# Kernel tuning notes

Hardware: AMD Instinct MI355X
Metric: run time of the kernel (lower is better)

The kernel has to match this reference:

```python
import jax, jax.numpy as jnp
import numpy as np

B, S, D = 4, 2048, 1024

def setup_inputs() -> dict:
    key = jax.random.key(0)
    ks = jax.random.split(key, 9)
    sc = 1.0 / np.sqrt(D)
    return {
        "x": jax.random.normal(ks[0], (B, S, D), dtype=jnp.float32),
        "Wq": jax.random.normal(ks[1], (D, D), dtype=jnp.float32) * sc,
        "bq": jnp.zeros((D,), dtype=jnp.float32),
        "Wk": jax.random.normal(ks[2], (D, D), dtype=jnp.float32) * sc,
        "bk": jnp.zeros((D,), dtype=jnp.float32),
        "Wv": jax.random.normal(ks[3], (D, D), dtype=jnp.float32) * sc,
        "bv": jnp.zeros((D,), dtype=jnp.float32),
        "Wo": jax.random.normal(ks[4], (D, D), dtype=jnp.float32) * sc,
        "bo": jnp.zeros((D,), dtype=jnp.float32),
    }

def _gaussian_mask(seq_len, dtype):
    # exp(-0.5*((pos - S/2)/(S/4))^2), shape [1,1,S] -> broadcasts over KEY axis
    pos = jnp.arange(seq_len, dtype=dtype)
    center = seq_len / 2
    sigma = seq_len / 4
    m = jnp.exp(-0.5 * ((pos - center) / sigma) ** 2)
    return m[None, None, :]

def reference(x, Wq, bq, Wk, bk, Wv, bv, Wo, bo):
    d = x.shape[-1]
    Q = x @ Wq.T + bq            # [B,S,D]
    K = x @ Wk.T + bk
    V = x @ Wv.T + bv
    scores = jnp.einsum('bqd,bkd->bqk', Q, K) / jnp.sqrt(jnp.asarray(d, x.dtype))
    scores = scores * _gaussian_mask(x.shape[1], x.dtype)
    attn = jax.nn.softmax(scores, axis=-1)
    out = jnp.einsum('bqk,bkd->bqd', attn, V)
    return out @ Wo.T + bo
```

## Files before the change

kernel.cpp:

```cpp
#include <hip/hip_runtime.h>
#include <math.h>

#define SEQ 2048
#define DIM 1024

typedef __attribute__((ext_vector_type(8))) _Float16 half8;
typedef __attribute__((ext_vector_type(4))) float f32x4;

__device__ __forceinline__ unsigned short f2h(float f) {
    union { _Float16 h; unsigned short u; } c; c.h = (_Float16)f;
    return c.u;
}
__device__ __forceinline__ float gmask(int k) {
    float t = ((float)k - 1024.0f) * (1.0f / 512.0f);
    return expf(-0.5f * t * t);
}
__device__ __forceinline__ void glds16(const unsigned short* gp, unsigned short* lp) {
    __builtin_amdgcn_global_load_lds((const __attribute__((address_space(1))) void*)gp,
                                     (__attribute__((address_space(3))) void*)lp, 16, 0, 0);
}

__device__ __forceinline__ void stage64(const unsigned short* __restrict__ g, int ldK,
                                        unsigned short* lds, int wave, int lane) {
    int row = wave * 32 + (lane >> 3);
    int seg = (lane & 7) ^ (lane >> 3);
    const unsigned short* gp = g + (long)row * ldK + seg * 8;
    unsigned short* lp = lds + wave * 2048;
    glds16(gp, lp);
    glds16(gp + 8 * (long)ldK, lp + 512);
    glds16(gp + 16 * (long)ldK, lp + 1024);
    glds16(gp + 24 * (long)ldK, lp + 1536);
}

enum { EPI_QKV = 0, EPI_EXP = 1, EPI_PV = 2, EPI_OUT = 3 };

template <int EPI>
__global__ __launch_bounds__(256, 2) void mfma_gemm(
    const unsigned short* __restrict__ A, const unsigned short* __restrict__ Bm,
    const float* __restrict__ bias, const float* __restrict__ rs,
    float* __restrict__ Cf, unsigned short* __restrict__ Ch,
    int M, int N, int K, float scale, long sA, long sB, long sC)
{
    __shared__ unsigned short As[128 * 64];
    __shared__ unsigned short Bs[128 * 64];

    const int bz = blockIdx.z;
    const int tid = threadIdx.x;
    const int wave = tid >> 6;
    const int lane = tid & 63;
    const int wm = (wave & 1) * 64;
    const int wn = (wave >> 1) * 64;
    const long m0 = (long)blockIdx.y * 128;
    const long n0 = (long)blockIdx.x * 128;
    const int lm = lane & 15;
    const int lk = lane >> 4;

    const unsigned short* pA = A + bz * sA + m0 * K;
    const unsigned short* pB = Bm + bz * sB + n0 * K;

    f32x4 acc[4][4];
#pragma unroll
    for (int i = 0; i < 4; ++i)
#pragma unroll
        for (int j = 0; j < 4; ++j) {
            acc[i][j].x = 0.f; acc[i][j].y = 0.f; acc[i][j].z = 0.f; acc[i][j].w = 0.f;
        }

    int aoff[4][2], boff[4][2];
#pragma unroll
    for (int i = 0; i < 4; ++i)
#pragma unroll
        for (int t = 0; t < 2; ++t) {
            int ar = wm + i * 16 + lm;
            aoff[i][t] = ar * 64 + (((4 * t + lk) ^ (ar & 7)) << 3);
            int br = wn + i * 16 + lm;
            boff[i][t] = br * 64 + (((4 * t + lk) ^ (br & 7)) << 3);
        }

    for (int k0 = 0; k0 < K; k0 += 64) {
        stage64(pA + k0, K, As, wave, lane);
        stage64(pB + k0, K, Bs, wave, lane);
        __syncthreads();
#pragma unroll
        for (int t = 0; t < 2; ++t) {
            half8 a[4], b[4];
#pragma unroll
            for (int i = 0; i < 4; ++i) a[i] = *(const half8*)(As + aoff[i][t]);
#pragma unroll
            for (int j = 0; j < 4; ++j) b[j] = *(const half8*)(Bs + boff[j][t]);
#pragma unroll
            for (int i = 0; i < 4; ++i)
#pragma unroll
                for (int j = 0; j < 4; ++j)
                    acc[i][j] = __builtin_amdgcn_mfma_f32_16x16x32_f16(a[i], b[j], acc[i][j], 0, 0, 0);
        }
        __syncthreads();
    }

    const long MD = 8388608;
    const float* rsb = (EPI == EPI_PV) ? rs + bz * SEQ : (const float*)nullptr;
    float* cF = (EPI == EPI_OUT) ? Cf + bz * sC : (float*)nullptr;
    unsigned short* cH = (EPI != EPI_OUT) ? Ch + bz * sC : (unsigned short*)nullptr;

#pragma unroll
    for (int i = 0; i < 4; ++i) {
        long mrow = m0 + wm + i * 16 + lk * 4;
        float rs4[4];
        if (EPI == EPI_PV) {
#pragma unroll
            for (int r = 0; r < 4; ++r) rs4[r] = rsb[mrow + r];
        }
#pragma unroll
        for (int j = 0; j < 4; ++j) {
            int n = (int)n0 + wn + j * 16 + lm;
            if (EPI == EPI_QKV) {
                int sel = n >> 10;
                int n1 = n & 1023;
                float bs = bias[n];
                if (sel < 2) {
                    unsigned short* dst = cH + (long)sel * MD;
#pragma unroll
                    for (int r = 0; r < 4; ++r)
                        dst[(mrow + r) * (long)DIM + n1] = f2h(acc[i][j][r] + bs);
                } else {
                    long b = mrow >> 11, s = mrow & 2047;
                    long idx = 2 * MD + b * (long)DIM * SEQ + (long)n1 * SEQ + s;
                    unsigned long long pk =
                        (unsigned long long)f2h(acc[i][j].x + bs) |
                        ((unsigned long long)f2h(acc[i][j].y + bs) << 16) |
                        ((unsigned long long)f2h(acc[i][j].z + bs) << 32) |
                        ((unsigned long long)f2h(acc[i][j].w + bs) << 48);
                    *(unsigned long long*)(cH + idx) = pk;
                }
            } else if (EPI == EPI_EXP) {
                float mult = scale * gmask(n);
#pragma unroll
                for (int r = 0; r < 4; ++r)
                    cH[(mrow + r) * (long)N + n] = f2h(expf(acc[i][j][r] * mult));
            } else if (EPI == EPI_PV) {
#pragma unroll
                for (int r = 0; r < 4; ++r)
                    cH[(mrow + r) * (long)N + n] = f2h(acc[i][j][r] * rs4[r]);
            } else {
                float bs = bias[n];
#pragma unroll
                for (int r = 0; r < 4; ++r)
                    cF[(mrow + r) * (long)N + n] = acc[i][j][r] + bs;
            }
        }
    }
}

__global__ __launch_bounds__(256) void rowsum(const unsigned short* __restrict__ E,
                                              float* __restrict__ invrs)
{
    long base = ((long)blockIdx.y * SEQ + blockIdx.x) * SEQ;
    const int tid = threadIdx.x;
    half8 h = ((const half8*)(E + base))[tid];
    float s = 0.f;
#pragma unroll
    for (int i = 0; i < 8; ++i) s += (float)h[i];
#pragma unroll
    for (int off = 32; off > 0; off >>= 1) s += __shfl_down(s, off);
    __shared__ float red[4];
    if ((tid & 63) == 0) red[tid >> 6] = s;
    __syncthreads();
    if (tid == 0)
        invrs[(long)blockIdx.y * SEQ + blockIdx.x] = 1.0f / (red[0] + red[1] + red[2] + red[3]);
}

__global__ __launch_bounds__(256) void cvt_f16(const float* __restrict__ src,
    unsigned short* __restrict__ dst, long n)
{
    long i = ((long)blockIdx.x * 256 + threadIdx.x) * 4;
    long stride = (long)gridDim.x * 1024;
    for (; i < n; i += stride) {
        float4 v = *(const float4*)(src + i);
        unsigned long long p = (unsigned long long)f2h(v.x) | ((unsigned long long)f2h(v.y) << 16) |
                               ((unsigned long long)f2h(v.z) << 32) | ((unsigned long long)f2h(v.w) << 48);
        *(unsigned long long*)(dst + i) = p;
    }
}

__global__ __launch_bounds__(256) void pack_w4(const float* __restrict__ W0,
    const float* __restrict__ W1, const float* __restrict__ W2, const float* __restrict__ W3,
    unsigned short* __restrict__ dst)
{
    const long WW = 1048576;
    long i = ((long)blockIdx.x * 256 + threadIdx.x) * 4;
    int sel = (int)(i >> 20);
    const float* src = (sel == 0) ? W0 : (sel == 1) ? W1 : (sel == 2) ? W2 : W3;
    float4 v = *(const float4*)(src + (i & (WW - 1)));
    unsigned long long p = (unsigned long long)f2h(v.x) | ((unsigned long long)f2h(v.y) << 16) |
                           ((unsigned long long)f2h(v.z) << 32) | ((unsigned long long)f2h(v.w) << 48);
    *(unsigned long long*)(dst + i) = p;
}

__global__ __launch_bounds__(256) void pack_bias(const float* __restrict__ b0,
    const float* __restrict__ b1, const float* __restrict__ b2, float* __restrict__ dst)
{
    int i = blockIdx.x * 256 + threadIdx.x;
    int sel = i >> 10;
    const float* src = (sel == 0) ? b0 : (sel == 1) ? b1 : b2;
    dst[i] = src[i & 1023];
}

extern "C" void kernel_launch(void* const* d_in, const int* in_sizes, int n_in,
                              void* d_out, int out_size, void* d_ws, size_t ws_size,
                              hipStream_t stream)
{
    const float* x  = (const float*)d_in[0];
    const float* Wq = (const float*)d_in[1];
    const float* bq = (const float*)d_in[2];
    const float* Wk = (const float*)d_in[3];
    const float* bk = (const float*)d_in[4];
    const float* Wv = (const float*)d_in[5];
    const float* bv = (const float*)d_in[6];
    const float* Wo = (const float*)d_in[7];
    const float* bo = (const float*)d_in[8];
    float* out = (float*)d_out;

    const long MD = 4L * SEQ * DIM;
    const long WW = (long)DIM * DIM;
    const long SD = (long)SEQ * DIM, SS = (long)SEQ * SEQ;

    unsigned short* xh   = (unsigned short*)d_ws;
    unsigned short* Wp   = xh + MD;
    unsigned short* Woh  = Wp + 3 * WW;
    float* bqkv          = (float*)(Wp + 4 * WW);
    unsigned short* Qh   = (unsigned short*)(bqkv + 4096);
    unsigned short* Kh   = Qh + MD;
    unsigned short* VT   = Kh + MD;
    unsigned short* expS = VT + MD;
    float* invrs         = (float*)(expS + 4L * SEQ * SEQ);
    unsigned short* O1   = xh;

    dim3 blk(256);
    cvt_f16<<<1024, blk, 0, stream>>>(x, xh, MD);
    pack_w4<<<4096, blk, 0, stream>>>(Wq, Wk, Wv, Wo, Wp);
    pack_bias<<<12, blk, 0, stream>>>(bq, bk, bv, bqkv);

    mfma_gemm<EPI_QKV><<<dim3(3 * DIM / 128, (4 * SEQ) / 128, 1), blk, 0, stream>>>(
        xh, Wp, bqkv, nullptr, nullptr, Qh, 4 * SEQ, 3 * DIM, DIM, 1.0f, 0, 0, 0);
    mfma_gemm<EPI_EXP><<<dim3(SEQ / 128, SEQ / 128, 4), blk, 0, stream>>>(
        Qh, Kh, nullptr, nullptr, nullptr, expS, SEQ, SEQ, DIM, 0.03125f, SD, SD, SS);
    rowsum<<<dim3(SEQ, 4), blk, 0, stream>>>(expS, invrs);
    mfma_gemm<EPI_PV><<<dim3(DIM / 128, SEQ / 128, 4), blk, 0, stream>>>(
        expS, VT, nullptr, invrs, nullptr, O1, SEQ, DIM, SEQ, 1.0f, SS, (long)DIM * SEQ, SD);
    mfma_gemm<EPI_OUT><<<dim3(DIM / 128, (4 * SEQ) / 128, 1), blk, 0, stream>>>(
        O1, Woh, bo, nullptr, out, nullptr, 4 * SEQ, DIM, DIM, 1.0f, 0, 0, 0);
}
```

Before: 295.4 us.

## Fuse softmax rowsum into PV GEMM and switch to 32x32 MFMA tiles

Removes the separate rowsum kernel by accumulating each row's sum of exponentials from the staged LDS A-tiles inside the PV GEMM, then normalizing in the epilogue. Switches the GEMM inner loop from 16x16x32 to 32x32x16 MFMA to cut LDS fragment loads per FLOP. Merges the three input conversion kernels into a single prep kernel to save launches. The rowsum work is repeated redundantly across the N-blocks of the PV GEMM, which adds some LDS reads and ALU work per block.

After: 295.4 us. About the same (+0.0%).

```diff
diff --git a/kernel.cpp b/kernel.cpp
--- a/kernel.cpp
+++ b/kernel.cpp
@@ -5,7 +5,7 @@
 #define DIM 1024
 
 typedef __attribute__((ext_vector_type(8))) _Float16 half8;
-typedef __attribute__((ext_vector_type(4))) float f32x4;
+typedef __attribute__((ext_vector_type(16))) float f32x16;
 
 __device__ __forceinline__ unsigned short f2h(float f) {
     union { _Float16 h; unsigned short u; } c; c.h = (_Float16)f;
@@ -37,7 +37,7 @@
 template <int EPI>
 __global__ __launch_bounds__(256, 2) void mfma_gemm(
     const unsigned short* __restrict__ A, const unsigned short* __restrict__ Bm,
-    const float* __restrict__ bias, const float* __restrict__ rs,
+    const float* __restrict__ bias,
     float* __restrict__ Cf, unsigned short* __restrict__ Ch,
     int M, int N, int K, float scale, long sA, long sB, long sC)
 {
@@ -52,157 +52,167 @@
     const int wn = (wave >> 1) * 64;
     const long m0 = (long)blockIdx.y * 128;
     const long n0 = (long)blockIdx.x * 128;
-    const int lm = lane & 15;
-    const int lk = lane >> 4;
+    const int l31 = lane & 31;
+    const int hk = lane >> 5;
 
     const unsigned short* pA = A + bz * sA + m0 * K;
     const unsigned short* pB = Bm + bz * sB + n0 * K;
 
-    f32x4 acc[4][4];
-#pragma unroll
-    for (int i = 0; i < 4; ++i)
-#pragma unroll
-        for (int j = 0; j < 4; ++j) {
-            acc[i][j].x = 0.f; acc[i][j].y = 0.f; acc[i][j].z = 0.f; acc[i][j].w = 0.f;
-        }
-
-    int aoff[4][2], boff[4][2];
-#pragma unroll
-    for (int i = 0; i < 4; ++i)
-#pragma unroll
-        for (int t = 0; t < 2; ++t) {
-            int ar = wm + i * 16 + lm;
-            aoff[i][t] = ar * 64 + (((4 * t + lk) ^ (ar & 7)) << 3);
-            int br = wn + i * 16 + lm;
-            boff[i][t] = br * 64 + (((4 * t + lk) ^ (br & 7)) << 3);
-        }
+    f32x16 acc[2][2];
+#pragma unroll
+    for (int i = 0; i < 2; ++i)
+#pragma unroll
+        for (int j = 0; j < 2; ++j)
+#pragma unroll
+            for (int e = 0; e < 16; ++e) acc[i][j][e] = 0.f;
+
+    int aoff[2][4], boff[2][4];
+#pragma unroll
+    for (int i = 0; i < 2; ++i)
+#pragma unroll
+        for (int t = 0; t < 4; ++t) {
+            int ar = wm + i * 32 + l31;
+            aoff[i][t] = ar * 64 + (((2 * t + hk) ^ (ar & 7)) << 3);
+            int br = wn + i * 32 + l31;
+            boff[i][t] = br * 64 + (((2 * t + hk) ^ (br & 7)) << 3);
+        }
+
+    const int pr = (wave & 1) * 64 + lane;
+    const int ph = wave >> 1;
+    float psum = 0.f;
 
     for (int k0 = 0; k0 < K; k0 += 64) {
         stage64(pA + k0, K, As, wave, lane);
         stage64(pB + k0, K, Bs, wave, lane);
         __syncthreads();
-#pragma unroll
-        for (int t = 0; t < 2; ++t) {
-            half8 a[4], b[4];
-#pragma unroll
-            for (int i = 0; i < 4; ++i) a[i] = *(const half8*)(As + aoff[i][t]);
-#pragma unroll
-            for (int j = 0; j < 4; ++j) b[j] = *(const half8*)(Bs + boff[j][t]);
-#pragma unroll
-            for (int i = 0; i < 4; ++i)
-#pragma unroll
-                for (int j = 0; j < 4; ++j)
-                    acc[i][j] = __builtin_amdgcn_mfma_f32_16x16x32_f16(a[i], b[j], acc[i][j], 0, 0, 0);
+
+        if (EPI == EPI_PV) {
+            const unsigned short* rowp = As + pr * 64;
+#pragma unroll
+            for (int i2 = 0; i2 < 4; ++i2) {
+                half8 h = *(const half8*)(rowp + (((2 * i2 + ph) ^ (pr & 7)) << 3));
+#pragma unroll
+                for (int e = 0; e < 8; ++e) psum += (float)h[e];
+            }
+        }
+
+#pragma unroll
+        for (int t = 0; t < 4; ++t) {
+            half8 a[2], b[2];
+#pragma unroll
+            for (int i = 0; i < 2; ++i) a[i] = *(const half8*)(As + aoff[i][t]);
+#pragma unroll
+            for (int j = 0; j < 2; ++j) b[j] = *(const half8*)(Bs + boff[j][t]);
+#pragma unroll
+            for (int i = 0; i < 2; ++i)
+#pragma unroll
+                for (int j = 0; j < 2; ++j)
+                    acc[i][j] = __builtin_amdgcn_mfma_f32_32x32x16_f16(a[i], b[j], acc[i][j], 0, 0, 0);
         }
         __syncthreads();
     }
 
+    float* rsf = (float*)As;
+    if (EPI == EPI_PV) {
+        rsf[ph * 128 + pr] = psum;
+        __syncthreads();
+    }
+
     const long MD = 8388608;
-    const float* rsb = (EPI == EPI_PV) ? rs + bz * SEQ : (const float*)nullptr;
     float* cF = (EPI == EPI_OUT) ? Cf + bz * sC : (float*)nullptr;
     unsigned short* cH = (EPI != EPI_OUT) ? Ch + bz * sC : (unsigned short*)nullptr;
 
-#pragma unroll
-    for (int i = 0; i < 4; ++i) {
-        long mrow = m0 + wm + i * 16 + lk * 4;
-        float rs4[4];
-        if (EPI == EPI_PV) {
-#pragma unroll
-            for (int r = 0; r < 4; ++r) rs4[r] = rsb[mrow + r];
-        }
-#pragma unroll
-        for (int j = 0; j < 4; ++j) {
-            int n = (int)n0 + wn + j * 16 + lm;
-            if (EPI == EPI_QKV) {
-                int sel = n >> 10;
-                int n1 = n & 1023;
-                float bs = bias[n];
-                if (sel < 2) {
-                    unsigned short* dst = cH + (long)sel * MD;
+    float bs_j[2], mult_j[2];
+#pragma unroll
+    for (int j = 0; j < 2; ++j) {
+        int n = (int)n0 + wn + j * 32 + l31;
+        if (EPI == EPI_QKV || EPI == EPI_OUT) bs_j[j] = bias[n];
+        if (EPI == EPI_EXP) mult_j[j] = scale * gmask(n);
+    }
+
+#pragma unroll
+    for (int i = 0; i < 2; ++i) {
+#pragma unroll
+        for (int q = 0; q < 4; ++q) {
+            long mrow = m0 + wm + i * 32 + q * 8 + hk * 4;
+            int lr = wm + i * 32 + q * 8 + hk * 4;
+            float inv4[4];
+            if (EPI == EPI_PV) {
+#pragma unroll
+                for (int r = 0; r < 4; ++r)
+                    inv4[r] = 1.0f / (rsf[lr + r] + rsf[128 + lr + r]);
+            }
+#pragma unroll
+            for (int j = 0; j < 2; ++j) {
+                int n = (int)n0 + wn + j * 32 + l31;
+                if (EPI == EPI_QKV) {
+                    int sel = n >> 10;
+                    int n1 = n & 1023;
+                    float bs = bs_j[j];
+                    if (sel < 2) {
+                        unsigned short* dst = cH + (long)sel * MD;
+#pragma unroll
+                        for (int r = 0; r < 4; ++r)
+                            dst[(mrow + r) * (long)DIM + n1] = f2h(acc[i][j][4 * q + r] + bs);
+                    } else {
+                        long b = mrow >> 11, s = mrow & 2047;
+                        long idx = 2 * MD + b * (long)DIM * SEQ + (long)n1 * SEQ + s;
+                        unsigned long long pk =
+                            (unsigned long long)f2h(acc[i][j][4 * q + 0] + bs) |
+                            ((unsigned long long)f2h(acc[i][j][4 * q + 1] + bs) << 16) |
+                            ((unsigned long long)f2h(acc[i][j][4 * q + 2] + bs) << 32) |
+                            ((unsigned long long)f2h(acc[i][j][4 * q + 3] + bs) << 48);
+                        *(unsigned long long*)(cH + idx) = pk;
+                    }
+                } else if (EPI == EPI_EXP) {
 #pragma unroll
                     for (int r = 0; r < 4; ++r)
-                        dst[(mrow + r) * (long)DIM + n1] = f2h(acc[i][j][r] + bs);
+                        cH[(mrow + r) * (long)N + n] = f2h(expf(acc[i][j][4 * q + r] * mult_j[j]));
+                } else if (EPI == EPI_PV) {
+#pragma unroll
+                    for (int r = 0; r < 4; ++r)
+                        cH[(mrow + r) * (long)N + n] = f2h(acc[i][j][4 * q + r] * inv4[r]);
                 } else {
-                    long b = mrow >> 11, s = mrow & 2047;
-                    long idx = 2 * MD + b * (long)DIM * SEQ + (long)n1 * SEQ + s;
-                    unsigned long long pk =
-                        (unsigned long long)f2h(acc[i][j].x + bs) |
-                        ((unsigned long long)f2h(acc[i][j].y + bs) << 16) |
-                        ((unsigned long long)f2h(acc[i][j].z + bs) << 32) |
-                        ((unsigned long long)f2h(acc[i][j].w + bs) << 48);
-                    *(unsigned long long*)(cH + idx) = pk;
+#pragma unroll
+                    for (int r = 0; r < 4; ++r)
+                        cF[(mrow + r) * (long)N + n] = acc[i][j][4 * q + r] + bs_j[j];
                 }
-            } else if (EPI == EPI_EXP) {
-                float mult = scale * gmask(n);
-#pragma unroll
-                for (int r = 0; r < 4; ++r)
-                    cH[(mrow + r) * (long)N + n] = f2h(expf(acc[i][j][r] * mult));
-            } else if (EPI == EPI_PV) {
-#pragma unroll
-                for (int r = 0; r < 4; ++r)
-                    cH[(mrow + r) * (long)N + n] = f2h(acc[i][j][r] * rs4[r]);
-            } else {
-                float bs = bias[n];
-#pragma unroll
-                for (int r = 0; r < 4; ++r)
-                    cF[(mrow + r) * (long)N + n] = acc[i][j][r] + bs;
             }
         }
     }
 }
 
-__global__ __launch_bounds__(256) void rowsum(const unsigned short* __restrict__ E,
-                                              float* __restrict__ invrs)
+__global__ __launch_bounds__(256) void prep(
+    const float* __restrict__ x,
+    const float* __restrict__ Wq, const float* __restrict__ Wk,
+    const float* __restrict__ Wv, const float* __restrict__ Wo,
+    const float* __restrict__ b0, const float* __restrict__ b1, const float* __restrict__ b2,
+    unsigned short* __restrict__ xh, unsigned short* __restrict__ Wp, float* __restrict__ bqkv)
 {
-    long base = ((long)blockIdx.y * SEQ + blockIdx.x) * SEQ;
-    const int tid = threadIdx.x;
-    half8 h = ((const half8*)(E + base))[tid];
-    float s = 0.f;
-#pragma unroll
-    for (int i = 0; i < 8; ++i) s += (float)h[i];
-#pragma unroll
-    for (int off = 32; off > 0; off >>= 1) s += __shfl_down(s, off);
-    __shared__ float red[4];
-    if ((tid & 63) == 0) red[tid >> 6] = s;
-    __syncthreads();
-    if (tid == 0)
-        invrs[(long)blockIdx.y * SEQ + blockIdx.x] = 1.0f / (red[0] + red[1] + red[2] + red[3]);
-}
-
-__global__ __launch_bounds__(256) void cvt_f16(const float* __restrict__ src,
-    unsigned short* __restrict__ dst, long n)
-{
-    long i = ((long)blockIdx.x * 256 + threadIdx.x) * 4;
-    long stride = (long)gridDim.x * 1024;
-    for (; i < n; i += stride) {
-        float4 v = *(const float4*)(src + i);
+    long gid = (long)blockIdx.x * 256 + threadIdx.x;
+    if (gid < 3072) {
+        int sel = (int)(gid >> 10);
+        const float* s = sel == 0 ? b0 : sel == 1 ? b1 : b2;
+        bqkv[gid] = s[gid & 1023];
+    }
+    const long NX = 8388608 / 4;
+    const long NW = 1048576 / 4;
+    const long total = NX + 4 * NW;
+    for (long i = gid; i < total; i += (long)gridDim.x * 256) {
+        const float* src; unsigned short* dst; long off;
+        if (i < NX) { src = x; dst = xh; off = i; }
+        else {
+            long wi = i - NX;
+            int sel = (int)(wi >> 18);
+            src = sel == 0 ? Wq : sel == 1 ? Wk : sel == 2 ? Wv : Wo;
+            dst = Wp + ((long)sel << 20);
+            off = wi & (NW - 1);
+        }
+        float4 v = ((const float4*)src)[off];
         unsigned long long p = (unsigned long long)f2h(v.x) | ((unsigned long long)f2h(v.y) << 16) |
                                ((unsigned long long)f2h(v.z) << 32) | ((unsigned long long)f2h(v.w) << 48);
-        *(unsigned long long*)(dst + i) = p;
-    }
-}
-
-__global__ __launch_bounds__(256) void pack_w4(const float* __restrict__ W0,
-    const float* __restrict__ W1, const float* __restrict__ W2, const float* __restrict__ W3,
-    unsigned short* __restrict__ dst)
-{
-    const long WW = 1048576;
-    long i = ((long)blockIdx.x * 256 + threadIdx.x) * 4;
-    int sel = (int)(i >> 20);
-    const float* src = (sel == 0) ? W0 : (sel == 1) ? W1 : (sel == 2) ? W2 : W3;
-    float4 v = *(const float4*)(src + (i & (WW - 1)));
-    unsigned long long p = (unsigned long long)f2h(v.x) | ((unsigned long long)f2h(v.y) << 16) |
-                           ((unsigned long long)f2h(v.z) << 32) | ((unsigned long long)f2h(v.w) << 48);
-    *(unsigned long long*)(dst + i) = p;
-}
-
-__global__ __launch_bounds__(256) void pack_bias(const float* __restrict__ b0,
-    const float* __restrict__ b1, const float* __restrict__ b2, float* __restrict__ dst)
-{
-    int i = blockIdx.x * 256 + threadIdx.x;
-    int sel = i >> 10;
-    const float* src = (sel == 0) ? b0 : (sel == 1) ? b1 : b2;
-    dst[i] = src[i & 1023];
+        ((unsigned long long*)dst)[off] = p;
+    }
 }
 
 extern "C" void kernel_launch(void* const* d_in, const int* in_sizes, int n_in,
@@ -229,24 +239,19 @@
     unsigned short* Woh  = Wp + 3 * WW;
     float* bqkv          = (float*)(Wp + 4 * WW);
     unsigned short* Qh   = (unsigned short*)(bqkv + 4096);
-    unsigned short* Kh   = Qh + MD;
-    unsigned short* VT   = Kh + MD;
-    unsigned short* expS = VT + MD;
-    float* invrs         = (float*)(expS + 4L * SEQ * SEQ);
+    unsigned short* VT   = Qh + 2 * MD;
+    unsigned short* expS = Qh + 3 * MD;
     unsigned short* O1   = xh;
 
     dim3 blk(256);
-    cvt_f16<<<1024, blk, 0, stream>>>(x, xh, MD);
-    pack_w4<<<4096, blk, 0, stream>>>(Wq, Wk, Wv, Wo, Wp);
-    pack_bias<<<12, blk, 0, stream>>>(bq, bk, bv, bqkv);
+    prep<<<4096, blk, 0, stream>>>(x, Wq, Wk, Wv, Wo, bq, bk, bv, xh, Wp, bqkv);
 
     mfma_gemm<EPI_QKV><<<dim3(3 * DIM / 128, (4 * SEQ) / 128, 1), blk, 0, stream>>>(
-        xh, Wp, bqkv, nullptr, nullptr, Qh, 4 * SEQ, 3 * DIM, DIM, 1.0f, 0, 0, 0);
+        xh, Wp, bqkv, nullptr, Qh, 4 * SEQ, 3 * DIM, DIM, 1.0f, 0, 0, 0);
     mfma_gemm<EPI_EXP><<<dim3(SEQ / 128, SEQ / 128, 4), blk, 0, stream>>>(
-        Qh, Kh, nullptr, nullptr, nullptr, expS, SEQ, SEQ, DIM, 0.03125f, SD, SD, SS);
-    rowsum<<<dim3(SEQ, 4), blk, 0, stream>>>(expS, invrs);
+        Qh, Qh + MD, nullptr, nullptr, expS, SEQ, SEQ, DIM, 0.03125f, SD, SD, SS);
     mfma_gemm<EPI_PV><<<dim3(DIM / 128, SEQ / 128, 4), blk, 0, stream>>>(
-        expS, VT, nullptr, invrs, nullptr, O1, SEQ, DIM, SEQ, 1.0f, SS, (long)DIM * SEQ, SD);
+        expS, VT, nullptr, nullptr, O1, SEQ, DIM, SEQ, 1.0f, SS, (long)DIM * SEQ, SD);
     mfma_gemm<EPI_OUT><<<dim3(DIM / 128, (4 * SEQ) / 128, 1), blk, 0, stream>>>(
-        O1, Woh, bo, nullptr, out, nullptr, 4 * SEQ, DIM, DIM, 1.0f, 0, 0, 0);
-}
+        O1, Woh, bo, out, nullptr, 4 * SEQ, DIM, DIM, 1.0f, 0, 0, 0);
+}
```
